# Optimization experiments

Measured on AMD Instinct MI355X. Metric: run time of the kernel, lower is better.

The kernel has to match this reference:

```python
import jax, jax.numpy as jnp
import numpy as np

SCORE_THRESHOLD = 0.5
GRID = 512  # spatial extent per axis; batch in {0,1} so keys fit int32
SENTINEL = np.int32(2 ** 30)  # larger than any real key (< 2**28)


def _encode(coords):
    # coords: [N,4] int32 (batch, x, y, z) -> unique int32 key
    c = coords.astype(jnp.int32)
    return ((c[:, 0] * GRID + c[:, 1]) * GRID + c[:, 2]) * GRID + c[:, 3]


def _decode_np(k):
    z = k % GRID; k = k // GRID
    y = k % GRID; k = k // GRID
    x = k % GRID; b = k // GRID
    return np.stack([b, x, y, z], axis=1).astype(np.int32)


def setup_inputs() -> dict:
    rng = np.random.default_rng(0)
    Nx, Nm, Dx = 2_000_000, 2_000_000, 16
    # draw unique coordinate keys (MinkowskiEngine coords are unique per tensor)
    keys = np.unique(rng.integers(0, 2 * GRID ** 3, size=3 * Nx, dtype=np.int64)).astype(np.int32)
    rng.shuffle(keys)
    x_keys = keys[:Nx]
    m_keys = np.concatenate([x_keys[: Nm // 2], keys[Nx: Nx + Nm - Nm // 2]])
    rng.shuffle(m_keys)
    key = jax.random.key(0)
    k1, k2 = jax.random.split(key)
    return {
        "x_C": jnp.asarray(_decode_np(x_keys)),
        "x_F": jax.random.normal(k1, (Nx, Dx), dtype=jnp.float32),
        "m_C": jnp.asarray(_decode_np(m_keys)),
        "m_F": jax.random.uniform(k2, (Nm, 1), dtype=jnp.float32),
    }


def _gather_on_union(keys, feats, union_keys):
    # scatter each tensor's features onto the union coordinate set (zeros elsewhere)
    n = keys.shape[0]
    order = jnp.argsort(keys)
    ks = keys[order]
    fs = feats[order]
    pos = jnp.searchsorted(ks, union_keys)
    pc = jnp.clip(pos, 0, n - 1)
    found = (pos < n) & (ks[pc] == union_keys)
    return jnp.where(found[:, None], fs[pc], jnp.zeros((), feats.dtype))


def reference(x_C, x_F, m_C, m_F):
    Nx, Nm = x_F.shape[0], m_F.shape[0]
    xk = _encode(x_C)
    mk = _encode(m_C)
    # coordinate union (ME sparse-tensor addition); fixed size Nx+Nm, padded w/ sentinel
    uk = jnp.unique(jnp.concatenate([xk, mk]), size=Nx + Nm, fill_value=SENTINEL)
    xf = _gather_on_union(xk, x_F, uk)   # x features on union coords  [Nu, Dx]
    mf = _gather_on_union(mk, m_F, uk)   # mask scores on union coords [Nu, 1]
    # target = score above threshold AND x has any positive feature at this coord
    target = (mf[:, 0] > SCORE_THRESHOLD) & (xf > 0).any(axis=1)
    # prune expressed as fixed-shape masking (padding rows have target=False)
    return xf * target[:, None].astype(xf.dtype)
```

## Files before the change

### kernel.cpp

```cpp
#include <hip/hip_runtime.h>
#include <hip/hip_bf16.h>
#include <stdint.h>

#define KEYSPACE   (1u << 28)
#define NWORDS     (KEYSPACE / 16u)
#define GROUP_W    16u
#define NGROUPS    (NWORDS / GROUP_W)
#define NSCANBLK   (NGROUPS / 1024u)
#define UMASK      0x55555555u

__device__ __forceinline__ uint32_t encode4(int4 c) {
    return ((((uint32_t)c.x * 512u + (uint32_t)c.y) * 512u + (uint32_t)c.z) * 512u) + (uint32_t)c.w;
}

__global__ __launch_bounds__(256) void mark_all(const int* __restrict__ xC,
                                                const int* __restrict__ mC,
                                                const float* __restrict__ mF,
                                                uint32_t* __restrict__ BM,
                                                int Nx, int Nm) {
    int i = blockIdx.x * blockDim.x + threadIdx.x;
    if (i < Nx) {
        int4 c = reinterpret_cast<const int4*>(xC)[i];
        uint32_t k = encode4(c);
        atomicOr(&BM[k >> 4], 1u << ((k & 15u) * 2u));
    } else {
        int j = i - Nx;
        if (j >= Nm) return;
        int4 c = reinterpret_cast<const int4*>(mC)[j];
        uint32_t k = encode4(c);
        uint32_t bits = (mF[j] > 0.5f) ? 3u : 1u;
        atomicOr(&BM[k >> 4], bits << ((k & 15u) * 2u));
    }
}

__global__ __launch_bounds__(256) void scan_blocks(const uint32_t* __restrict__ BM,
                                                   uint32_t* __restrict__ P,
                                                   uint32_t* __restrict__ B) {
    __shared__ uint32_t sdata[256];
    int t = threadIdx.x;
    uint32_t blk = blockIdx.x;
    size_t g0 = (size_t)blk * 1024u + (uint32_t)t * 4u;
    const uint4* p = reinterpret_cast<const uint4*>(BM) + g0 * 4u;
    uint32_t cg[4];
#pragma unroll
    for (int q = 0; q < 4; ++q) {
        uint4 a = p[q * 4 + 0], b = p[q * 4 + 1], c = p[q * 4 + 2], d = p[q * 4 + 3];
        cg[q] = __popc(a.x & UMASK) + __popc(a.y & UMASK) + __popc(a.z & UMASK) + __popc(a.w & UMASK)
              + __popc(b.x & UMASK) + __popc(b.y & UMASK) + __popc(b.z & UMASK) + __popc(b.w & UMASK)
              + __popc(c.x & UMASK) + __popc(c.y & UMASK) + __popc(c.z & UMASK) + __popc(c.w & UMASK)
              + __popc(d.x & UMASK) + __popc(d.y & UMASK) + __popc(d.z & UMASK) + __popc(d.w & UMASK);
    }
    uint32_t s = cg[0] + cg[1] + cg[2] + cg[3];
    sdata[t] = s;
    __syncthreads();
    for (int off = 1; off < 256; off <<= 1) {
        uint32_t tmp = (t >= off) ? sdata[t - off] : 0u;
        __syncthreads();
        sdata[t] += tmp;
        __syncthreads();
    }
    uint32_t ex = sdata[t] - s;
    uint4 o;
    o.x = ex;
    o.y = ex + cg[0];
    o.z = ex + cg[0] + cg[1];
    o.w = ex + cg[0] + cg[1] + cg[2];
    reinterpret_cast<uint4*>(P)[blk * 256u + t] = o;
    if (t == 255) B[blk] = sdata[255];
}

__global__ __launch_bounds__(1024) void scan_top(const uint32_t* __restrict__ B,
                                                 uint32_t* __restrict__ Boff) {
    __shared__ uint32_t sdata[1024];
    int t = threadIdx.x;
    uint32_t v = B[t];
    sdata[t] = v;
    __syncthreads();
    for (int off = 1; off < 1024; off <<= 1) {
        uint32_t tmp = (t >= off) ? sdata[t - off] : 0u;
        __syncthreads();
        sdata[t] += tmp;
        __syncthreads();
    }
    Boff[t] = sdata[t] - v;
}

__global__ __launch_bounds__(256) void scatter_rows(const int* __restrict__ xC,
                                                    const float* __restrict__ xF,
                                                    const uint32_t* __restrict__ BM,
                                                    const uint32_t* __restrict__ P,
                                                    const uint32_t* __restrict__ Boff,
                                                    float* __restrict__ out, int Nx) {
    int i = blockIdx.x * blockDim.x + threadIdx.x;
    if (i >= Nx) return;
    int4 c = reinterpret_cast<const int4*>(xC)[i];
    uint32_t k = encode4(c);
    uint32_t w = k >> 4;
    uint32_t j2 = (k & 15u) * 2u;
    uint32_t word = BM[w];
    if (!((word >> (j2 + 1u)) & 1u)) return;

    const float4* f = reinterpret_cast<const float4*>(xF + (size_t)i * 16u);
    float4 f0 = f[0], f1 = f[1], f2 = f[2], f3 = f[3];
    bool any =
        (f0.x > 0.f) | (f0.y > 0.f) | (f0.z > 0.f) | (f0.w > 0.f) |
        (f1.x > 0.f) | (f1.y > 0.f) | (f1.z > 0.f) | (f1.w > 0.f) |
        (f2.x > 0.f) | (f2.y > 0.f) | (f2.z > 0.f) | (f2.w > 0.f) |
        (f3.x > 0.f) | (f3.y > 0.f) | (f3.z > 0.f) | (f3.w > 0.f);
    if (!any) return;

    uint32_t g = w >> 4;
    uint32_t r = Boff[g >> 10] + P[g];
    for (uint32_t q = g << 4; q < w; ++q) r += __popc(BM[q] & UMASK);
    r += __popc(word & UMASK & ((1u << j2) - 1u));

    float4* o = reinterpret_cast<float4*>(out + (size_t)r * 16u);
    o[0] = f0; o[1] = f1; o[2] = f2; o[3] = f3;
}

extern "C" void kernel_launch(void* const* d_in, const int* in_sizes, int n_in,
                              void* d_out, int out_size, void* d_ws, size_t ws_size,
                              hipStream_t stream) {
    const int* xC = (const int*)d_in[0];
    const float* xF = (const float*)d_in[1];
    const int* mC = (const int*)d_in[2];
    const float* mF = (const float*)d_in[3];
    float* out = (float*)d_out;

    int Nx = in_sizes[1] / 16;
    int Nm = in_sizes[3];

    uint8_t* ws = (uint8_t*)d_ws;
    uint32_t* BM   = (uint32_t*)(ws);
    uint32_t* P    = (uint32_t*)(ws + (size_t)64 * 1024 * 1024);
    uint32_t* B    = (uint32_t*)(ws + (size_t)68 * 1024 * 1024);
    uint32_t* Boff = (uint32_t*)(ws + (size_t)68 * 1024 * 1024 + 4096);

    hipMemsetAsync(BM, 0, (size_t)64 * 1024 * 1024, stream);
    hipMemsetAsync(out, 0, (size_t)out_size * sizeof(float), stream);

    int blk = 256;
    int total = Nx + Nm;
    mark_all<<<(total + blk - 1) / blk, blk, 0, stream>>>(xC, mC, mF, BM, Nx, Nm);
    scan_blocks<<<NSCANBLK, 256, 0, stream>>>(BM, P, B);
    scan_top<<<1, 1024, 0, stream>>>(B, Boff);
    scatter_rows<<<(Nx + blk - 1) / blk, blk, 0, stream>>>(xC, xF, BM, P, Boff, out, Nx);
}
```

Before: 594.9 us.

## Replace global bitmap with bucketed binning and per-bucket shared-memory bitmaps

Drops the 64 MB global bitmap, its memset, and the full scan over it. Keys are first binned into 2048 buckets by their high bits. Each bucket then builds a small bitmap and prefix in LDS and computes union ranks for x rows that pass the mask score. A final gather kernel copies the qualifying rows to their ranked positions. This avoids the large global memset and scan, but adds a two-pass binning step and fixed-capacity buckets (4096 entries) and record buffers (1024 per bucket) that could overflow on skewed inputs.

```diff
diff --git a/kernel.cpp b/kernel.cpp
--- a/kernel.cpp
+++ b/kernel.cpp
@@ -2,55 +2,108 @@
 #include <hip/hip_bf16.h>
 #include <stdint.h>
 
-#define KEYSPACE   (1u << 28)
-#define NWORDS     (KEYSPACE / 16u)
-#define GROUP_W    16u
-#define NGROUPS    (NWORDS / GROUP_W)
-#define NSCANBLK   (NGROUPS / 1024u)
-#define UMASK      0x55555555u
+#define KEYSPACE     (1u << 28)
+#define NBUCKET      2048u
+#define BUCKET_KEYS  (KEYSPACE / NBUCKET)
+#define BUCKET_WORDS (BUCKET_KEYS / 16u)
+#define BUCKET_CAP   4096u
+#define EPB          16384
+#define UMASK        0x55555555u
+#define RECS_CAP     1024u
 
 __device__ __forceinline__ uint32_t encode4(int4 c) {
     return ((((uint32_t)c.x * 512u + (uint32_t)c.y) * 512u + (uint32_t)c.z) * 512u) + (uint32_t)c.w;
 }
 
-__global__ __launch_bounds__(256) void mark_all(const int* __restrict__ xC,
+__global__ __launch_bounds__(256) void bin_keys(const int* __restrict__ xC,
                                                 const int* __restrict__ mC,
                                                 const float* __restrict__ mF,
-                                                uint32_t* __restrict__ BM,
+                                                uint2* __restrict__ barr,
+                                                uint32_t* __restrict__ bcnt,
                                                 int Nx, int Nm) {
-    int i = blockIdx.x * blockDim.x + threadIdx.x;
-    if (i < Nx) {
-        int4 c = reinterpret_cast<const int4*>(xC)[i];
-        uint32_t k = encode4(c);
-        atomicOr(&BM[k >> 4], 1u << ((k & 15u) * 2u));
-    } else {
-        int j = i - Nx;
-        if (j >= Nm) return;
-        int4 c = reinterpret_cast<const int4*>(mC)[j];
-        uint32_t k = encode4(c);
-        uint32_t bits = (mF[j] > 0.5f) ? 3u : 1u;
-        atomicOr(&BM[k >> 4], bits << ((k & 15u) * 2u));
-    }
-}
-
-__global__ __launch_bounds__(256) void scan_blocks(const uint32_t* __restrict__ BM,
-                                                   uint32_t* __restrict__ P,
-                                                   uint32_t* __restrict__ B) {
+    __shared__ uint32_t hist[NBUCKET];
+    __shared__ uint32_t base[NBUCKET];
+    int t = threadIdx.x;
+    int total = Nx + Nm;
+    int start = blockIdx.x * EPB;
+    int end = min(start + EPB, total);
+
+    for (int q = t; q < (int)NBUCKET; q += 256) hist[q] = 0u;
+    __syncthreads();
+
+    for (int e = start + t; e < end; e += 256) {
+        uint32_t k = (e < Nx) ? encode4(reinterpret_cast<const int4*>(xC)[e])
+                              : encode4(reinterpret_cast<const int4*>(mC)[e - Nx]);
+        atomicAdd(&hist[k >> 17], 1u);
+    }
+    __syncthreads();
+
+    for (int q = t; q < (int)NBUCKET; q += 256) {
+        uint32_t h = hist[q];
+        base[q] = h ? atomicAdd(&bcnt[q], h) : 0u;
+        hist[q] = 0u;
+    }
+    __syncthreads();
+
+    for (int e = start + t; e < end; e += 256) {
+        uint32_t k; uint2 pl;
+        if (e < Nx) {
+            k = encode4(reinterpret_cast<const int4*>(xC)[e]);
+            pl.x = (k & (BUCKET_KEYS - 1u)) | (1u << 18);
+            pl.y = (uint32_t)e;
+        } else {
+            int j = e - Nx;
+            k = encode4(reinterpret_cast<const int4*>(mC)[j]);
+            pl.x = (k & (BUCKET_KEYS - 1u)) | ((mF[j] > 0.5f) ? (1u << 17) : 0u);
+            pl.y = 0u;
+        }
+        uint32_t b = k >> 17;
+        uint32_t pos = base[b] + atomicAdd(&hist[b], 1u);
+        barr[(size_t)b * BUCKET_CAP + pos] = pl;
+    }
+}
+
+__global__ __launch_bounds__(256) void build_bucket(const uint2* __restrict__ barr,
+                                                    const uint32_t* __restrict__ bcnt,
+                                                    uint2* __restrict__ records,
+                                                    uint32_t* __restrict__ rcount,
+                                                    uint32_t* __restrict__ Btot) {
+    __shared__ uint32_t bmp[BUCKET_WORDS];
+    __shared__ uint32_t gpre[512];
     __shared__ uint32_t sdata[256];
+    __shared__ uint2 recs[RECS_CAP];
+    __shared__ uint32_t nrec, rbase;
     int t = threadIdx.x;
-    uint32_t blk = blockIdx.x;
-    size_t g0 = (size_t)blk * 1024u + (uint32_t)t * 4u;
-    const uint4* p = reinterpret_cast<const uint4*>(BM) + g0 * 4u;
-    uint32_t cg[4];
+    uint32_t b = blockIdx.x;
+
+    {
+        uint4 z = make_uint4(0u, 0u, 0u, 0u);
+        uint4* bz = reinterpret_cast<uint4*>(bmp);
+        for (int q = t; q < (int)(BUCKET_WORDS / 4u); q += 256) bz[q] = z;
+    }
+    __syncthreads();
+
+    uint32_t n = bcnt[b];
+    const uint2* ba = barr + (size_t)b * BUCKET_CAP;
+
+    for (uint32_t e = t; e < n; e += 256u) {
+        uint32_t pl = ba[e].x;
+        uint32_t off = pl & (BUCKET_KEYS - 1u);
+        uint32_t bits = 1u | (((pl >> 17) & 1u) << 1);
+        atomicOr(&bmp[off >> 4], bits << ((off & 15u) * 2u));
+    }
+    __syncthreads();
+
+    uint32_t c0 = 0u, c1 = 0u;
+    {
+        const uint32_t* w0 = bmp + (2 * t) * 16;
+        const uint32_t* w1 = bmp + (2 * t + 1) * 16;
 #pragma unroll
-    for (int q = 0; q < 4; ++q) {
-        uint4 a = p[q * 4 + 0], b = p[q * 4 + 1], c = p[q * 4 + 2], d = p[q * 4 + 3];
-        cg[q] = __popc(a.x & UMASK) + __popc(a.y & UMASK) + __popc(a.z & UMASK) + __popc(a.w & UMASK)
-              + __popc(b.x & UMASK) + __popc(b.y & UMASK) + __popc(b.z & UMASK) + __popc(b.w & UMASK)
-              + __popc(c.x & UMASK) + __popc(c.y & UMASK) + __popc(c.z & UMASK) + __popc(c.w & UMASK)
-              + __popc(d.x & UMASK) + __popc(d.y & UMASK) + __popc(d.z & UMASK) + __popc(d.w & UMASK);
-    }
-    uint32_t s = cg[0] + cg[1] + cg[2] + cg[3];
+        for (int q = 0; q < 16; ++q) c0 += __popc(w0[q] & UMASK);
+#pragma unroll
+        for (int q = 0; q < 16; ++q) c1 += __popc(w1[q] & UMASK);
+    }
+    uint32_t s = c0 + c1;
     sdata[t] = s;
     __syncthreads();
     for (int off = 1; off < 256; off <<= 1) {
@@ -60,21 +113,42 @@
         __syncthreads();
     }
     uint32_t ex = sdata[t] - s;
-    uint4 o;
-    o.x = ex;
-    o.y = ex + cg[0];
-    o.z = ex + cg[0] + cg[1];
-    o.w = ex + cg[0] + cg[1] + cg[2];
-    reinterpret_cast<uint4*>(P)[blk * 256u + t] = o;
-    if (t == 255) B[blk] = sdata[255];
-}
-
-__global__ __launch_bounds__(1024) void scan_top(const uint32_t* __restrict__ B,
+    gpre[2 * t] = ex;
+    gpre[2 * t + 1] = ex + c0;
+    if (t == 255) Btot[b] = sdata[255];
+    if (t == 0) nrec = 0u;
+    __syncthreads();
+
+    for (uint32_t e = t; e < n; e += 256u) {
+        uint2 pe = ba[e];
+        if (!(pe.x & (1u << 18))) continue;
+        uint32_t off = pe.x & (BUCKET_KEYS - 1u);
+        uint32_t w = off >> 4;
+        uint32_t j2 = (off & 15u) * 2u;
+        uint32_t word = bmp[w];
+        if (!((word >> (j2 + 1u)) & 1u)) continue;
+        uint32_t g = off >> 8;
+        uint32_t r = gpre[g];
+        for (uint32_t q = g << 4; q < w; ++q) r += __popc(bmp[q] & UMASK);
+        r += __popc(word & UMASK & ((1u << j2) - 1u));
+        uint32_t pos = atomicAdd(&nrec, 1u);
+        if (pos < RECS_CAP) recs[pos] = make_uint2(pe.y, (b << 17) | r);
+    }
+    __syncthreads();
+
+    if (t == 0) rbase = atomicAdd(rcount, min(nrec, RECS_CAP));
+    __syncthreads();
+    uint32_t n2 = min(nrec, RECS_CAP);
+    for (uint32_t q = t; q < n2; q += 256u) records[rbase + q] = recs[q];
+}
+
+__global__ __launch_bounds__(1024) void scan_top(const uint32_t* __restrict__ Btot,
                                                  uint32_t* __restrict__ Boff) {
     __shared__ uint32_t sdata[1024];
     int t = threadIdx.x;
-    uint32_t v = B[t];
-    sdata[t] = v;
+    uint32_t v0 = Btot[2 * t], v1 = Btot[2 * t + 1];
+    uint32_t s = v0 + v1;
+    sdata[t] = s;
     __syncthreads();
     for (int off = 1; off < 1024; off <<= 1) {
         uint32_t tmp = (t >= off) ? sdata[t - off] : 0u;
@@ -82,25 +156,23 @@
         sdata[t] += tmp;
         __syncthreads();
     }
-    Boff[t] = sdata[t] - v;
-}
-
-__global__ __launch_bounds__(256) void scatter_rows(const int* __restrict__ xC,
-                                                    const float* __restrict__ xF,
-                                                    const uint32_t* __restrict__ BM,
-                                                    const uint32_t* __restrict__ P,
-                                                    const uint32_t* __restrict__ Boff,
-                                                    float* __restrict__ out, int Nx) {
-    int i = blockIdx.x * blockDim.x + threadIdx.x;
-    if (i >= Nx) return;
-    int4 c = reinterpret_cast<const int4*>(xC)[i];
-    uint32_t k = encode4(c);
-    uint32_t w = k >> 4;
-    uint32_t j2 = (k & 15u) * 2u;
-    uint32_t word = BM[w];
-    if (!((word >> (j2 + 1u)) & 1u)) return;
-
-    const float4* f = reinterpret_cast<const float4*>(xF + (size_t)i * 16u);
+    uint32_t ex = sdata[t] - s;
+    Boff[2 * t] = ex;
+    Boff[2 * t + 1] = ex + v0;
+}
+
+__global__ __launch_bounds__(256) void gather_rows(const uint2* __restrict__ records,
+                                                   const uint32_t* __restrict__ rcount,
+                                                   const uint32_t* __restrict__ Boff,
+                                                   const float* __restrict__ xF,
+                                                   float* __restrict__ out) {
+    uint32_t i = blockIdx.x * blockDim.x + threadIdx.x;
+    if (i >= *rcount) return;
+    uint2 rec = records[i];
+    uint32_t row = rec.x;
+    uint32_t r = Boff[rec.y >> 17] + (rec.y & (BUCKET_KEYS - 1u));
+
+    const float4* f = reinterpret_cast<const float4*>(xF + (size_t)row * 16u);
     float4 f0 = f[0], f1 = f[1], f2 = f[2], f3 = f[3];
     bool any =
         (f0.x > 0.f) | (f0.y > 0.f) | (f0.z > 0.f) | (f0.w > 0.f) |
@@ -108,11 +180,6 @@
         (f2.x > 0.f) | (f2.y > 0.f) | (f2.z > 0.f) | (f2.w > 0.f) |
         (f3.x > 0.f) | (f3.y > 0.f) | (f3.z > 0.f) | (f3.w > 0.f);
     if (!any) return;
-
-    uint32_t g = w >> 4;
-    uint32_t r = Boff[g >> 10] + P[g];
-    for (uint32_t q = g << 4; q < w; ++q) r += __popc(BM[q] & UMASK);
-    r += __popc(word & UMASK & ((1u << j2) - 1u));
 
     float4* o = reinterpret_cast<float4*>(out + (size_t)r * 16u);
     o[0] = f0; o[1] = f1; o[2] = f2; o[3] = f3;
@@ -129,20 +196,21 @@
 
     int Nx = in_sizes[1] / 16;
     int Nm = in_sizes[3];
+    int total = Nx + Nm;
 
     uint8_t* ws = (uint8_t*)d_ws;
-    uint32_t* BM   = (uint32_t*)(ws);
-    uint32_t* P    = (uint32_t*)(ws + (size_t)64 * 1024 * 1024);
-    uint32_t* B    = (uint32_t*)(ws + (size_t)68 * 1024 * 1024);
-    uint32_t* Boff = (uint32_t*)(ws + (size_t)68 * 1024 * 1024 + 4096);
-
-    hipMemsetAsync(BM, 0, (size_t)64 * 1024 * 1024, stream);
+    uint2*    barr    = (uint2*)(ws);
+    uint2*    records = (uint2*)(ws + (size_t)64 * 1024 * 1024);
+    uint32_t* bcnt    = (uint32_t*)(ws + (size_t)80 * 1024 * 1024);
+    uint32_t* rcount  = (uint32_t*)(ws + (size_t)80 * 1024 * 1024 + 8192);
+    uint32_t* Btot    = (uint32_t*)(ws + (size_t)80 * 1024 * 1024 + 12288);
+    uint32_t* Boff    = (uint32_t*)(ws + (size_t)80 * 1024 * 1024 + 20480);
+
     hipMemsetAsync(out, 0, (size_t)out_size * sizeof(float), stream);
-
-    int blk = 256;
-    int total = Nx + Nm;
-    mark_all<<<(total + blk - 1) / blk, blk, 0, stream>>>(xC, mC, mF, BM, Nx, Nm);
-    scan_blocks<<<NSCANBLK, 256, 0, stream>>>(BM, P, B);
-    scan_top<<<1, 1024, 0, stream>>>(B, Boff);
-    scatter_rows<<<(Nx + blk - 1) / blk, blk, 0, stream>>>(xC, xF, BM, P, Boff, out, Nx);
-}
+    hipMemsetAsync(bcnt, 0, 8192 + 4, stream);
+
+    bin_keys<<<(total + EPB - 1) / EPB, 256, 0, stream>>>(xC, mC, mF, barr, bcnt, Nx, Nm);
+    build_bucket<<<NBUCKET, 256, 0, stream>>>(barr, bcnt, records, rcount, Btot);
+    scan_top<<<1, 1024, 0, stream>>>(Btot, Boff);
+    gather_rows<<<(Nx + 255) / 256, 256, 0, stream>>>(records, rcount, Boff, xF, out);
+}
```

New measurement: 547.3 us. 1.09x faster.
